# Kernel tuning notes

Measured on AMD Instinct MI355X. Metric: run time of the kernel, lower is better.

Reference implementation:

```python
import jax, jax.numpy as jnp
import numpy as np

SCALE = 32.0      # backbone feature->image coordinate scale (stride)
LOG_EPS = 1e-8    # geometry.safe_log epsilon


def _safe_log(x):
    return jnp.log(jnp.maximum(x, LOG_EPS))


def setup_inputs() -> dict:
    key = jax.random.key(0)
    k1, k2, k3, k4, k5, k6 = jax.random.split(key, 6)
    B, P, L = 128, 4096, 128
    cls_scores = jax.random.normal(k1, (B, 2 * P), dtype=jnp.float32)
    bbox_deltas = jax.random.normal(k2, (B, 4 * P), dtype=jnp.float32) * 0.1
    # RoI in feature coordinates: x,y in [0,40), w,h in [1,11)
    roi_xy = jax.random.uniform(k3, (B, P, 2), dtype=jnp.float32) * 40.0
    roi_wh = jax.random.uniform(k4, (B, P, 2), dtype=jnp.float32) * 10.0 + 1.0
    roi = jnp.concatenate([roi_xy, roi_wh], axis=-1)
    # Ground-truth labels in image coordinates: x,y in [0,1280), w,h in [32,352)
    lab_xy = jax.random.uniform(k5, (B, L, 2), dtype=jnp.float32) * 1280.0
    lab_wh = jax.random.uniform(k6, (B, L, 2), dtype=jnp.float32) * 320.0 + 32.0
    labels = jnp.concatenate([lab_xy, lab_wh], axis=-1)
    return {
        "cls_scores": cls_scores,
        "bbox_deltas": bbox_deltas,
        "roi": roi,
        "labels": labels,
        "neg_enabled": 1,
    }


def reference(cls_scores, bbox_deltas, roi, labels, neg_enabled):
    """Vectorized port of ClassifierModel._compute_loss summed over the batch.

    cls_scores  [B, 2P] laid out [class, proposal] (cls[i::P] -> per-proposal logits)
    bbox_deltas [B, 4P] laid out [coord, proposal]
    roi         [B, P, 4] proposals in feature coords (x,y,w,h)
    labels      [B, L, 4] ground-truth boxes in image coords (x,y,w,h)
    """
    B, P = roi.shape[0], roi.shape[1]
    roi_img = roi.astype(jnp.float32) * SCALE  # feature -> image coords

    # --- IoU matrix [B, L, P] (geometry.calculate_IoU over all label/proposal pairs)
    l = labels[:, :, None, :]   # [B, L, 1, 4]
    r = roi_img[:, None, :, :]  # [B, 1, P, 4]
    ix = jnp.maximum(0.0, jnp.minimum(l[..., 0] + l[..., 2], r[..., 0] + r[..., 2]) - jnp.maximum(l[..., 0], r[..., 0]))
    iy = jnp.maximum(0.0, jnp.minimum(l[..., 1] + l[..., 3], r[..., 1] + r[..., 3]) - jnp.maximum(l[..., 1], r[..., 1]))
    inter = ix * iy
    union = l[..., 2] * l[..., 3] + r[..., 2] * r[..., 3] - inter
    iou = jnp.where(union > 0.0, inter / union, 0.0)  # [B, L, P]

    # --- matching: argmax over labels where any IoU is nonzero, else -1
    any_hit = jnp.sum((iou != 0.0).astype(jnp.int32), axis=1) > 0        # [B, P]
    match = jnp.where(any_hit, jnp.argmax(iou, axis=1), -1)              # [B, P]
    pos = match > 0  # NOTE: original uses match[i] > 0 (strict), kept faithfully

    matched = jnp.take_along_axis(labels, jnp.clip(match, 0)[:, :, None], axis=1)  # [B, P, 4]
    tx = (matched[..., 0] - roi_img[..., 0]) / roi_img[..., 2]
    ty = (matched[..., 1] - roi_img[..., 1]) / roi_img[..., 3]
    tw = _safe_log(matched[..., 2] / roi_img[..., 2])
    th = _safe_log(matched[..., 3] / roi_img[..., 3])
    targets = jnp.stack([tx, ty, tw, th], axis=-1)                        # [B, P, 4]
    preds = bbox_deltas.reshape(B, 4, P).transpose(0, 2, 1)               # [B, P, 4]

    # Huber (delta=1, mean over the 4 coords) per proposal
    err = targets - preds
    ae = jnp.abs(err)
    huber = jnp.mean(jnp.where(ae <= 1.0, 0.5 * err * err, ae - 0.5), axis=-1)  # [B, P]

    # --- classification: softmax over the two per-proposal logits, then
    # CategoricalCrossentropy(probs, const) = -sum(probs * log(const))
    logits = cls_scores.reshape(B, 2, P).transpose(0, 2, 1)               # [B, P, 2]
    probs = jax.nn.softmax(logits, axis=-1)
    log_pos = jnp.log(jnp.array([0.1, 0.9], dtype=jnp.float32))
    log_neg = jnp.log(jnp.array([0.9, 0.1], dtype=jnp.float32))
    ce_pos = -jnp.sum(probs * log_pos, axis=-1)                           # [B, P]
    ce_neg = -jnp.sum(probs * log_neg, axis=-1)                           # [B, P]

    neg_term = jnp.where(jnp.asarray(neg_enabled) > 0, ce_neg, 0.0)
    per_prop = jnp.where(pos, 2.0 * huber + ce_pos, neg_term)             # [B, P]
    return jnp.sum(per_prop)
```

## Files before the change

### kernel.cpp

```cpp
#include <hip/hip_runtime.h>
#include <hip/hip_bf16.h>
#include <math.h>

#define BB 128
#define PP 4096
#define LL 128
#define BLOCK 256
#define PROPS 2
#define CHUNKS (PP / (BLOCK * PROPS))
#define SCALE 32.0f
#define LCHUNK 8

__global__ __launch_bounds__(256) void prep_areas_kernel(
    const float* __restrict__ labels, float* __restrict__ areas)
{
    int i = blockIdx.x * 256 + threadIdx.x;
    if (i < BB * LL)
        areas[i] = labels[(size_t)i * 4 + 2] * labels[(size_t)i * 4 + 3];
}

__global__ __launch_bounds__(BLOCK) void classifier_loss_kernel(
    const float* __restrict__ cls,
    const float* __restrict__ bbox,
    const float* __restrict__ roi,
    const float* __restrict__ labels,
    const float* __restrict__ areas,
    const int* __restrict__ neg_enabled,
    float* __restrict__ out)
{
    __shared__ float4 s_lab4[LL];
    __shared__ float  s_red[BLOCK / 64];

    const int b     = blockIdx.x >> 3;
    const int chunk = blockIdx.x & (CHUNKS - 1);
    const int pbase = chunk * (BLOCK * PROPS) + threadIdx.x;

    if (threadIdx.x < LL) {
        const float* lp = labels + ((size_t)b * LL + threadIdx.x) * 4;
        float x = lp[0], y = lp[1], w = lp[2], h = lp[3];
        s_lab4[threadIdx.x] = make_float4(x, y, x + w, y + h);
    }

    const float* __restrict__ ab = areas + (size_t)b * LL;

    float rx[PROPS], ry[PROPS], rx2[PROPS], ry2[PROPS], rarea[PROPS];
    float cs0[PROPS], cs1[PROPS];
    float bi[PROPS], bd[PROPS];
    int   bidx[PROPS];

    #pragma unroll
    for (int j = 0; j < PROPS; ++j) {
        const int p = pbase + j * BLOCK;
        const float* rp = roi + ((size_t)b * PP + p) * 4;
        float r0 = rp[0], r1 = rp[1], r2 = rp[2], r3 = rp[3];
        cs0[j] = cls[(size_t)b * 2 * PP + p];
        cs1[j] = cls[(size_t)b * 2 * PP + PP + p];
        rx[j]  = r0 * SCALE;
        ry[j]  = r1 * SCALE;
        float rw = r2 * SCALE, rh = r3 * SCALE;
        rx2[j] = rx[j] + rw;
        ry2[j] = ry[j] + rh;
        rarea[j] = rw * rh;
        bi[j] = -1.0f;
        bd[j] = 1.0f;
        bidx[j] = 0;
    }

    __syncthreads();

    for (int lc = 0; lc < LL; lc += LCHUNK) {
        #pragma unroll
        for (int u = 0; u < LCHUNK; ++u) {
            const int li = lc + u;
            const float4 l4 = s_lab4[li];
            const float s_area = ab[li];
            #pragma unroll
            for (int j = 0; j < PROPS; ++j) {
                float ix = fmaxf(0.0f, fminf(l4.z, rx2[j]) - fmaxf(l4.x, rx[j]));
                float iy = fmaxf(0.0f, fminf(l4.w, ry2[j]) - fmaxf(l4.y, ry[j]));
                float inter = ix * iy;
                float denom = s_area + rarea[j];
                bool gt = inter * bd[j] > bi[j] * denom;
                bi[j]   = gt ? inter : bi[j];
                bd[j]   = gt ? denom : bd[j];
                bidx[j] = gt ? li    : bidx[j];
            }
        }
    }

    const float LOG01 = -2.3025850929940457f;
    const float LOG09 = -0.10536051565782628f;
    const bool neg_on = neg_enabled[0] > 0;

    float acc = 0.0f;
    #pragma unroll
    for (int j = 0; j < PROPS; ++j) {
        const int p = pbase + j * BLOCK;
        const bool pos = (bi[j] > 0.0f) && (bidx[j] > 0);

        const float mx = fmaxf(cs0[j], cs1[j]);
        const float e0 = expf(cs0[j] - mx);
        const float e1 = expf(cs1[j] - mx);
        const float inv = 1.0f / (e0 + e1);
        const float p0 = e0 * inv, p1 = e1 * inv;
        const float ce_pos = -(p0 * LOG01 + p1 * LOG09);
        const float ce_neg = -(p0 * LOG09 + p1 * LOG01);

        float per;
        if (pos) {
            const float* mp = labels + ((size_t)b * LL + bidx[j]) * 4;
            float mxl = mp[0], myl = mp[1], mwl = mp[2], mhl = mp[3];
            float rw = rx2[j] - rx[j];
            float rh = ry2[j] - ry[j];
            float tx = (mxl - rx[j]) / rw;
            float ty = (myl - ry[j]) / rh;
            float tw = logf(fmaxf(mwl / rw, 1e-8f));
            float th = logf(fmaxf(mhl / rh, 1e-8f));
            const float* bp = bbox + (size_t)b * 4 * PP + p;
            float ex = tx - bp[0];
            float ey = ty - bp[PP];
            float ew = tw - bp[2 * PP];
            float eh = th - bp[3 * PP];
            float ax = fabsf(ex), ay = fabsf(ey), aw = fabsf(ew), ah = fabsf(eh);
            float hx = (ax <= 1.0f) ? 0.5f * ex * ex : ax - 0.5f;
            float hy = (ay <= 1.0f) ? 0.5f * ey * ey : ay - 0.5f;
            float hw = (aw <= 1.0f) ? 0.5f * ew * ew : aw - 0.5f;
            float hh = (ah <= 1.0f) ? 0.5f * eh * eh : ah - 0.5f;
            float huber = 0.25f * (hx + hy + hw + hh);
            per = 2.0f * huber + ce_pos;
        } else {
            per = neg_on ? ce_neg : 0.0f;
        }
        acc += per;
    }

    float v = acc;
    #pragma unroll
    for (int off = 32; off > 0; off >>= 1)
        v += __shfl_down(v, off, 64);
    if ((threadIdx.x & 63) == 0)
        s_red[threadIdx.x >> 6] = v;
    __syncthreads();
    if (threadIdx.x == 0) {
        float blk = s_red[0] + s_red[1] + s_red[2] + s_red[3];
        atomicAdd(out, blk);
    }
}

extern "C" void kernel_launch(void* const* d_in, const int* in_sizes, int n_in,
                              void* d_out, int out_size, void* d_ws, size_t ws_size,
                              hipStream_t stream) {
    const float* cls    = (const float*)d_in[0];
    const float* bbox   = (const float*)d_in[1];
    const float* roi    = (const float*)d_in[2];
    const float* labels = (const float*)d_in[3];
    const int*   neg    = (const int*)d_in[4];
    float* out   = (float*)d_out;
    float* areas = (float*)d_ws;

    hipMemsetAsync(out, 0, sizeof(float) * out_size, stream);
    prep_areas_kernel<<<dim3((BB * LL + 255) / 256), dim3(256), 0, stream>>>(
        labels, areas);
    classifier_loss_kernel<<<dim3(BB * PP / (BLOCK * PROPS)), dim3(BLOCK), 0, stream>>>(
        cls, bbox, roi, labels, areas, neg, out);
}
```

Measured before the change: 109.8 us.

## Pack label index into IoU low mantissa bits and use single fmax argmax

Replaces the cross-multiplied argmax (three selects per pair) with an approximate reciprocal ratio whose low 7 mantissa bits hold the inverted label index, so a single fmaxf tracks both best value and index. It also computes label areas inline, which removes the separate prep kernel and the global area loads, and drops one clamp on iy. The cost is precision: truncated mantissa bits and an approximate reciprocal can pick a different label on near-ties, and the positive test now uses a small threshold instead of strict > 0.

Measured after the change: 103.4 us. -5.9%, faster.

```diff
diff --git a/kernel.cpp b/kernel.cpp
--- a/kernel.cpp
+++ b/kernel.cpp
@@ -11,20 +11,11 @@
 #define SCALE 32.0f
 #define LCHUNK 8
 
-__global__ __launch_bounds__(256) void prep_areas_kernel(
-    const float* __restrict__ labels, float* __restrict__ areas)
-{
-    int i = blockIdx.x * 256 + threadIdx.x;
-    if (i < BB * LL)
-        areas[i] = labels[(size_t)i * 4 + 2] * labels[(size_t)i * 4 + 3];
-}
-
 __global__ __launch_bounds__(BLOCK) void classifier_loss_kernel(
     const float* __restrict__ cls,
     const float* __restrict__ bbox,
     const float* __restrict__ roi,
     const float* __restrict__ labels,
-    const float* __restrict__ areas,
     const int* __restrict__ neg_enabled,
     float* __restrict__ out)
 {
@@ -41,12 +32,9 @@
         s_lab4[threadIdx.x] = make_float4(x, y, x + w, y + h);
     }
 
-    const float* __restrict__ ab = areas + (size_t)b * LL;
-
     float rx[PROPS], ry[PROPS], rx2[PROPS], ry2[PROPS], rarea[PROPS];
     float cs0[PROPS], cs1[PROPS];
-    float bi[PROPS], bd[PROPS];
-    int   bidx[PROPS];
+    float best[PROPS];
 
     #pragma unroll
     for (int j = 0; j < PROPS; ++j) {
@@ -61,9 +49,7 @@
         rx2[j] = rx[j] + rw;
         ry2[j] = ry[j] + rh;
         rarea[j] = rw * rh;
-        bi[j] = -1.0f;
-        bd[j] = 1.0f;
-        bidx[j] = 0;
+        best[j] = 0.0f;
     }
 
     __syncthreads();
@@ -73,17 +59,16 @@
         for (int u = 0; u < LCHUNK; ++u) {
             const int li = lc + u;
             const float4 l4 = s_lab4[li];
-            const float s_area = ab[li];
+            const float S = (l4.z - l4.x) * (l4.w - l4.y);
             #pragma unroll
             for (int j = 0; j < PROPS; ++j) {
                 float ix = fmaxf(0.0f, fminf(l4.z, rx2[j]) - fmaxf(l4.x, rx[j]));
-                float iy = fmaxf(0.0f, fminf(l4.w, ry2[j]) - fmaxf(l4.y, ry[j]));
+                float iy = fminf(l4.w, ry2[j]) - fmaxf(l4.y, ry[j]);
                 float inter = ix * iy;
-                float denom = s_area + rarea[j];
-                bool gt = inter * bd[j] > bi[j] * denom;
-                bi[j]   = gt ? inter : bi[j];
-                bd[j]   = gt ? denom : bd[j];
-                bidx[j] = gt ? li    : bidx[j];
+                float denom = S + rarea[j];
+                float c = inter * __builtin_amdgcn_rcpf(denom);
+                unsigned kb = (__float_as_uint(c) & 0xFFFFFF80u) | (unsigned)(127 - li);
+                best[j] = fmaxf(best[j], __uint_as_float(kb));
             }
         }
     }
@@ -96,7 +81,8 @@
     #pragma unroll
     for (int j = 0; j < PROPS; ++j) {
         const int p = pbase + j * BLOCK;
-        const bool pos = (bi[j] > 0.0f) && (bidx[j] > 0);
+        const int bidx = 127 - (int)(__float_as_uint(best[j]) & 127u);
+        const bool pos = (best[j] > 1e-25f) && (bidx > 0);
 
         const float mx = fmaxf(cs0[j], cs1[j]);
         const float e0 = expf(cs0[j] - mx);
@@ -108,7 +94,7 @@
 
         float per;
         if (pos) {
-            const float* mp = labels + ((size_t)b * LL + bidx[j]) * 4;
+            const float* mp = labels + ((size_t)b * LL + bidx) * 4;
             float mxl = mp[0], myl = mp[1], mwl = mp[2], mhl = mp[3];
             float rw = rx2[j] - rx[j];
             float rh = ry2[j] - ry[j];
@@ -155,12 +141,9 @@
     const float* roi    = (const float*)d_in[2];
     const float* labels = (const float*)d_in[3];
     const int*   neg    = (const int*)d_in[4];
-    float* out   = (float*)d_out;
-    float* areas = (float*)d_ws;
+    float* out = (float*)d_out;
 
     hipMemsetAsync(out, 0, sizeof(float) * out_size, stream);
-    prep_areas_kernel<<<dim3((BB * LL + 255) / 256), dim3(256), 0, stream>>>(
-        labels, areas);
     classifier_loss_kernel<<<dim3(BB * PP / (BLOCK * PROPS)), dim3(BLOCK), 0, stream>>>(
-        cls, bbox, roi, labels, areas, neg, out);
+        cls, bbox, roi, labels, neg, out);
 }
```
